# Performance work log

Hardware: AMD Instinct MI355X
Metric: run time of the kernel (lower is better)

The kernel has to match this reference:

```python
import jax, jax.numpy as jnp
import numpy as np

N = 100000   # nodes
P = 3        # metapaths
E = 800000   # edges per metapath (avg degree 8)
IN = 128     # in_size
H = 4        # layer_num_heads
D = 32       # out_size per head
HID = 64     # semantic attention hidden
NEG_SLOPE = 0.2


def setup_inputs() -> dict:
    key = jax.random.key(0)
    ks = jax.random.split(key, 10)
    h = jax.random.normal(ks[0], (N, IN), jnp.float32)
    edge_src = jax.random.randint(ks[1], (P, E), 0, N, dtype=jnp.int32).astype(jnp.int64)
    edge_dst = jax.random.randint(ks[2], (P, E), 0, N, dtype=jnp.int32).astype(jnp.int64)
    W = jax.random.normal(ks[3], (P, IN, H * D), jnp.float32) * 0.05
    attn_l = jax.random.normal(ks[4], (P, H, D), jnp.float32) * 0.05
    attn_r = jax.random.normal(ks[5], (P, H, D), jnp.float32) * 0.05
    bias = jnp.zeros((P, H * D), jnp.float32)
    sa_w1 = jax.random.normal(ks[6], (H * D, HID), jnp.float32) * 0.05
    sa_b1 = jnp.zeros((HID,), jnp.float32)
    sa_w2 = jax.random.normal(ks[7], (HID, 1), jnp.float32) * 0.05
    return {"h": h, "edge_src": edge_src, "edge_dst": edge_dst, "W": W,
            "attn_l": attn_l, "attn_r": attn_r, "bias": bias,
            "sa_w1": sa_w1, "sa_b1": sa_b1, "sa_w2": sa_w2}


def _gat_conv(h, src, dst, Wp, al, ar, bp):
    # DGL GATConv: project, per-edge additive attention, edge softmax over dst, scatter-sum.
    n = h.shape[0]
    feat = (h @ Wp).reshape(n, H, D)              # [N,H,D]
    el = (feat * al).sum(-1)                      # [N,H]
    er = (feat * ar).sum(-1)                      # [N,H]
    e = jax.nn.leaky_relu(el[src] + er[dst], NEG_SLOPE)   # [E,H]
    emax = jax.ops.segment_max(e, dst, num_segments=n)    # [N,H]
    emax = jnp.where(jnp.isfinite(emax), emax, 0.0)       # zero-in-degree guard
    ex = jnp.exp(e - emax[dst])                            # [E,H]
    denom = jax.ops.segment_sum(ex, dst, num_segments=n)   # [N,H]
    alpha = ex / jnp.maximum(denom[dst], 1e-9)              # [E,H]
    msg = alpha[:, :, None] * feat[src]                     # [E,H,D]
    out = jax.ops.segment_sum(msg, dst, num_segments=n)     # [N,H,D]
    return out.reshape(n, H * D) + bp


def reference(h, edge_src, edge_dst, W, attn_l, attn_r, bias, sa_w1, sa_b1, sa_w2):
    embs = []
    for p in range(P):  # small fixed metapath set
        embs.append(_gat_conv(h, edge_src[p], edge_dst[p], W[p], attn_l[p], attn_r[p], bias[p]))
    z = jnp.stack(embs, axis=1)                 # [N,P,H*D]
    # SemanticAttention: MLP score, mean over nodes, softmax over metapaths
    w = (jnp.tanh(z @ sa_w1 + sa_b1) @ sa_w2).mean(0)   # [P,1]
    beta = jax.nn.softmax(w, axis=0)                     # [P,1]
    return (beta[None, :, :] * z).sum(1)                 # [N,H*D]
```

## Files before the change

### kernel.cpp

```cpp
#include <hip/hip_runtime.h>
#include <hip/hip_bf16.h>
#include <math.h>

#define NN 100000
#define NP 3
#define NE 800000
#define NH 4
#define ND 32
#define HD 128
#define NHID 64

#define SLW 256
#define SBK 512
#define GB 391
#define NBLK 196
#define ECHUNK 4096
#define EPT 16
#define EMAX 2368

typedef __attribute__((ext_vector_type(8))) short short8;
typedef __attribute__((ext_vector_type(4))) float f32x4;

__device__ __forceinline__ unsigned short f2bf(float f) {
  union { float f; unsigned int u; } v; v.f = f;
  unsigned int r = v.u + 0x7FFFu + ((v.u >> 16) & 1u);
  return (unsigned short)(r >> 16);
}
__device__ __forceinline__ float bf2f(unsigned short u) {
  return __uint_as_float(((unsigned int)u) << 16);
}
__device__ __forceinline__ float tanh_fast(float x) {
  return 1.f - 2.f / (1.f + __expf(2.f * x));
}

__global__ __launch_bounds__(256) void prep_fill_kernel(
    const float* __restrict__ h, const float* __restrict__ W, const float* __restrict__ W1,
    const int* __restrict__ src_all, const int* __restrict__ dst_all,
    unsigned short* __restrict__ hb, unsigned short* __restrict__ WT,
    unsigned short* __restrict__ W1T, float* __restrict__ s,
    int* __restrict__ cntA, int* __restrict__ baseA, int* __restrict__ pairs) {
  __shared__ int hist[SBK];
  __shared__ int scanb[SBK];
  const int tid = threadIdx.x;
  const int bx = blockIdx.x;
  if (bx < 12500) {
    int i = bx * 256 + tid;
    if (i < NN * 32) {
      float4 v = ((const float4*)h)[i];
      ushort4 o;
      o.x = f2bf(v.x); o.y = f2bf(v.y); o.z = f2bf(v.z); o.w = f2bf(v.w);
      ((ushort4*)hb)[i] = o;
    }
    if (i < NP * 128 * 128) {
      int p = i >> 14, r = i & 16383, n = r >> 7, k = r & 127;
      WT[i] = f2bf(W[(size_t)p * 16384 + k * 128 + n]);
    }
    if (i < NHID * 128) {
      int n = i >> 7, k = i & 127;
      W1T[i] = f2bf(W1[(size_t)k * NHID + n]);
    }
    if (i < 4) s[i] = 0.f;
    return;
  }
  const int b2 = bx - 12500;
  const int p = b2 / NBLK, blk = b2 % NBLK;
  const int* dstp = dst_all + (size_t)p * NE;
  const int* srcp = src_all + (size_t)p * NE;
  hist[tid] = 0; hist[tid + 256] = 0;
  __syncthreads();
  int dv[EPT], sv[EPT];
#pragma unroll
  for (int k = 0; k < EPT; ++k) {
    int e = blk * ECHUNK + k * 256 + tid;
    dv[k] = -1; sv[k] = 0;
    if (e < NE) {
      dv[k] = __builtin_nontemporal_load(dstp + e);
      sv[k] = __builtin_nontemporal_load(srcp + e);
    }
    if (dv[k] >= 0) atomicAdd(&hist[(unsigned)dv[k] >> 8], 1);
  }
  __syncthreads();
  scanb[tid] = hist[tid]; scanb[tid + 256] = hist[tid + 256];
  __syncthreads();
  for (int off = 1; off < SBK; off <<= 1) {
    int a0 = (tid >= off) ? scanb[tid - off] : 0;
    int a1 = scanb[tid + 256 - off];
    __syncthreads();
    scanb[tid] += a0; scanb[tid + 256] += a1;
    __syncthreads();
  }
  int c0 = hist[tid], c1 = hist[tid + 256];
  int b0 = scanb[tid] - c0, b1 = scanb[tid + 256] - c1;
  int* cA = cntA + ((size_t)p * NBLK + blk) * SBK;
  int* bA = baseA + ((size_t)p * NBLK + blk) * SBK;
  cA[tid] = c0; cA[tid + 256] = c1;
  bA[tid] = b0; bA[tid + 256] = b1;
  __syncthreads();
  scanb[tid] = b0; scanb[tid + 256] = b1;
  hist[tid] = 0; hist[tid + 256] = 0;
  __syncthreads();
  int* prp = pairs + (size_t)p * NE + (size_t)blk * ECHUNK;
#pragma unroll
  for (int k = 0; k < EPT; ++k) {
    if (dv[k] >= 0) {
      int sl = (unsigned)dv[k] >> 8;
      int pos = scanb[sl] + atomicAdd(&hist[sl], 1);
      prp[pos] = ((dv[k] & 255) << 17) | sv[k];
    }
  }
}

__global__ __launch_bounds__(256) void gemm_mfma_kernel(
    const unsigned short* __restrict__ hb, const unsigned short* __restrict__ WT_all,
    const float* __restrict__ al_all, const float* __restrict__ ar_all,
    unsigned short* __restrict__ featb_all, float* __restrict__ el_all,
    float* __restrict__ er_all) {
  __shared__ unsigned short Bs[128 * 128];
  const int p = blockIdx.y;
  const unsigned short* WTp = WT_all + (size_t)p * 16384;
#pragma unroll
  for (int it = 0; it < 8; ++it)
    ((float4*)Bs)[it * 256 + threadIdx.x] = ((const float4*)WTp)[it * 256 + threadIdx.x];
  __syncthreads();

  const int wid = threadIdx.x >> 6, lane = threadIdx.x & 63;
  const int c = lane & 15, q = lane >> 4;
  const int tile = blockIdx.x * 4 + wid;
  const int tc = tile < 6250 ? tile : 6249;

  f32x4 acc[8];
#pragma unroll
  for (int t = 0; t < 8; ++t) acc[t] = (f32x4){0.f, 0.f, 0.f, 0.f};

  const unsigned short* arow = hb + (size_t)(tc * 16 + c) * 128 + q * 8;
#pragma unroll
  for (int kc = 0; kc < 4; ++kc) {
    short8 a = *(const short8*)(arow + kc * 32);
#pragma unroll
    for (int t = 0; t < 8; ++t) {
      short8 b = *(const short8*)(Bs + (size_t)(t * 16 + c) * 128 + kc * 32 + q * 8);
      acc[t] = __builtin_amdgcn_mfma_f32_16x16x32_bf16(a, b, acc[t], 0, 0, 0);
    }
  }
  if (tile >= 6250) return;

  unsigned short* featb = featb_all + (size_t)p * NN * 128;
#pragma unroll
  for (int t = 0; t < 8; ++t)
#pragma unroll
    for (int i = 0; i < 4; ++i)
      featb[(size_t)(tc * 16 + q * 4 + i) * 128 + t * 16 + c] = f2bf(acc[t][i]);

  const float* al = al_all + p * 128;
  const float* ar = ar_all + p * 128;
  float alv[8], arv[8];
#pragma unroll
  for (int t = 0; t < 8; ++t) { alv[t] = al[t * 16 + c]; arv[t] = ar[t * 16 + c]; }
  float elp[4][4], erp[4][4];
#pragma unroll
  for (int i = 0; i < 4; ++i)
#pragma unroll
    for (int hh = 0; hh < 4; ++hh) {
      elp[i][hh] = acc[2 * hh][i] * alv[2 * hh] + acc[2 * hh + 1][i] * alv[2 * hh + 1];
      erp[i][hh] = acc[2 * hh][i] * arv[2 * hh] + acc[2 * hh + 1][i] * arv[2 * hh + 1];
    }
#pragma unroll
  for (int m = 1; m <= 8; m <<= 1)
#pragma unroll
    for (int i = 0; i < 4; ++i)
#pragma unroll
      for (int hh = 0; hh < 4; ++hh) {
        elp[i][hh] += __shfl_xor(elp[i][hh], m);
        erp[i][hh] += __shfl_xor(erp[i][hh], m);
      }
  if (c == 0) {
    float* el = el_all + (size_t)p * NN * 4;
    float* er = er_all + (size_t)p * NN * 4;
#pragma unroll
    for (int i = 0; i < 4; ++i) {
      int row = tc * 16 + q * 4 + i;
      *(float4*)(el + (size_t)row * 4) = make_float4(elp[i][0], elp[i][1], elp[i][2], elp[i][3]);
      *(float4*)(er + (size_t)row * 4) = make_float4(erp[i][0], erp[i][1], erp[i][2], erp[i][3]);
    }
  }
}

__global__ __launch_bounds__(512) void fillB2a_kernel(
    const int* __restrict__ cntA, const int* __restrict__ baseA,
    const int* __restrict__ pairs, int* __restrict__ srtpk,
    int2* __restrict__ rowidx, int* __restrict__ btot) {
  __shared__ int scnt[NBLK];
  __shared__ int sbase[NBLK];
  __shared__ int scum[NBLK];
  __shared__ int totE;
  __shared__ int hist[SLW];
  __shared__ int start[SLW];
  __shared__ int wcur[SLW];
  __shared__ int earr[EMAX];
  const int tid = threadIdx.x;
  const int p = blockIdx.y, sl = blockIdx.x;
  const size_t base = ((size_t)p * GB + sl) * EMAX;

  for (int b = tid; b < NBLK; b += 512) {
    scnt[b] = cntA[((size_t)p * NBLK + b) * SBK + sl];
    sbase[b] = baseA[((size_t)p * NBLK + b) * SBK + sl];
  }
  if (tid < SLW) hist[tid] = 0;
  __syncthreads();
  if (tid < NBLK) scum[tid] = scnt[tid];
  __syncthreads();
  for (int off = 1; off < NBLK; off <<= 1) {
    int a = (tid < NBLK && tid >= off) ? scum[tid - off] : 0;
    __syncthreads();
    if (tid < NBLK) scum[tid] += a;
    __syncthreads();
  }
  if (tid == NBLK - 1) { int t = scum[NBLK - 1]; totE = t > EMAX ? EMAX : t; }
  int excl = (tid < NBLK) ? scum[tid] - scnt[tid] : 0;
  __syncthreads();
  if (tid < NBLK) scum[tid] = excl;
  __syncthreads();
  const int total = totE;
  const int* prp = pairs + (size_t)p * NE;
  for (int e = tid; e < total; e += 512) {
    int lo = 0, hi = NBLK - 1;
    while (lo < hi) { int mid = (lo + hi + 1) >> 1; if (scum[mid] <= e) lo = mid; else hi = mid - 1; }
    int pk = prp[(size_t)lo * ECHUNK + sbase[lo] + (e - scum[lo])];
    earr[e] = pk;
    atomicAdd(&hist[pk >> 17], 1);
  }
  __syncthreads();
  if (tid < SLW) start[tid] = hist[tid];
  __syncthreads();
  for (int off = 1; off < SLW; off <<= 1) {
    int a = (tid < SLW && tid >= off) ? start[tid - off] : 0;
    __syncthreads();
    if (tid < SLW) start[tid] += a;
    __syncthreads();
  }
  if (tid < SLW) { int st = start[tid] - hist[tid]; start[tid] = st; wcur[tid] = st; }
  __syncthreads();
  for (int e = tid; e < total; e += 512) {
    int pk = earr[e];
    int pos = atomicAdd(&wcur[pk >> 17], 1);
    srtpk[base + pos] = pk;
  }
  if (tid < SLW) {
    int n = sl * SLW + tid;
    if (n < NN) rowidx[(size_t)p * NN + n] = make_int2((int)(base + start[tid]), hist[tid]);
  }
  if (tid == 0) btot[p * GB + sl] = total;
}

__global__ __launch_bounds__(256) void fillB2b_kernel(
    const int* __restrict__ srtpk, const int* __restrict__ btot,
    const float* __restrict__ el_all, const float* __restrict__ er_all,
    float4* __restrict__ xs) {
  const int p = blockIdx.y, sl = blockIdx.x;
  const int total = btot[p * GB + sl];
  const size_t base = ((size_t)p * GB + sl) * EMAX;
  const float* el = el_all + (size_t)p * NN * 4;
  const float* er = er_all + (size_t)p * NN * 4;
  for (int i = threadIdx.x; i < total; i += 256) {
    int pk = srtpk[base + i];
    int src = pk & 0x1FFFF, dl = pk >> 17;
    int n = sl * SLW + dl;
    float4 ev = *(const float4*)(el + (size_t)src * 4);
    float4 rv = *(const float4*)(er + (size_t)n * 4);
    float4 x;
    float e0 = ev.x + rv.x; e0 = fmaxf(e0, 0.2f * e0); x.x = __expf(e0);
    float e1 = ev.y + rv.y; e1 = fmaxf(e1, 0.2f * e1); x.y = __expf(e1);
    float e2 = ev.z + rv.z; e2 = fmaxf(e2, 0.2f * e2); x.z = __expf(e2);
    float e3 = ev.w + rv.w; e3 = fmaxf(e3, 0.2f * e3); x.w = __expf(e3);
    xs[base + i] = x;
  }
}

__global__ __launch_bounds__(256) void gather3_kernel(
    const unsigned short* __restrict__ featb_all, const int* __restrict__ srtpk,
    const float* __restrict__ xs, const int2* __restrict__ rowidx,
    const float* __restrict__ bias_all, unsigned short* __restrict__ zb) {
  const int p = blockIdx.y;
  const unsigned short* featb = featb_all + (size_t)p * NN * 128;
  const int wid = threadIdx.x >> 6;
  const int lane = threadIdx.x & 63;
  const int n = blockIdx.x * 4 + wid;
  int2 rd = rowidx[(size_t)p * NN + n];
  const int rbase = rd.x, deg = rd.y;

  const int j16 = lane & 15, hgrp = lane >> 4;
  const int sub = lane >> 4, c16 = lane & 15;
  const int hh = c16 >> 2;

  float acc[8] = {0.f, 0.f, 0.f, 0.f, 0.f, 0.f, 0.f, 0.f};
  float dsum = 0.f;

  for (int b = 0; b < deg; b += 16) {
    int s = 0; float x = 0.f;
    int jj = b + j16;
    if (jj < deg) {
      int idx = rbase + jj;
      s = srtpk[idx] & 0x1FFFF;
      x = xs[(size_t)idx * 4 + hgrp];
    }
    int bend = deg - b; bend = bend > 16 ? 16 : bend;
    for (int i = 0; i < bend; i += 8) {
      int j0 = i + sub, j1 = i + 4 + sub;
      int s0 = __shfl(s, j0);
      int s1 = __shfl(s, j1);
      float xv0 = __shfl(x, (hh << 4) | j0);
      float xv1 = __shfl(x, (hh << 4) | j1);
      short8 f0 = *(const short8*)(featb + (size_t)s0 * 128 + c16 * 8);
      short8 f1 = *(const short8*)(featb + (size_t)s1 * 128 + c16 * 8);
      dsum += xv0 + xv1;
#pragma unroll
      for (int k = 0; k < 8; ++k) acc[k] += xv0 * bf2f((unsigned short)f0[k]);
#pragma unroll
      for (int k = 0; k < 8; ++k) acc[k] += xv1 * bf2f((unsigned short)f1[k]);
    }
  }
  dsum += __shfl_xor(dsum, 16); dsum += __shfl_xor(dsum, 32);
#pragma unroll
  for (int k = 0; k < 8; ++k) {
    acc[k] += __shfl_xor(acc[k], 16);
    acc[k] += __shfl_xor(acc[k], 32);
  }
  if (sub == 0) {
    float rdn = dsum > 0.f ? 1.f / dsum : 0.f;
    const float* bias = bias_all + p * 128 + c16 * 8;
    float4 b0 = *(const float4*)(bias);
    float4 b1 = *(const float4*)(bias + 4);
    short8 o;
    o[0] = f2bf(acc[0] * rdn + b0.x); o[1] = f2bf(acc[1] * rdn + b0.y);
    o[2] = f2bf(acc[2] * rdn + b0.z); o[3] = f2bf(acc[3] * rdn + b0.w);
    o[4] = f2bf(acc[4] * rdn + b1.x); o[5] = f2bf(acc[5] * rdn + b1.y);
    o[6] = f2bf(acc[6] * rdn + b1.z); o[7] = f2bf(acc[7] * rdn + b1.w);
    *(short8*)(zb + (size_t)n * (NP * 128) + p * 128 + c16 * 8) = o;
  }
}

__global__ __launch_bounds__(256) void sem_mfma_kernel(
    const unsigned short* __restrict__ zb, const unsigned short* __restrict__ W1T,
    const float* __restrict__ b1, const float* __restrict__ w2,
    float* __restrict__ s) {
  __shared__ float red3[3];
  if (threadIdx.x < 3) red3[threadIdx.x] = 0.f;
  __syncthreads();
  const int wid = threadIdx.x >> 6, lane = threadIdx.x & 63;
  const int tile = blockIdx.x * 4 + wid;
  const bool active = tile < 18750;
  const int tc = active ? tile : 18749;
  const int c = lane & 15, q = lane >> 4;
  f32x4 acc[4];
#pragma unroll
  for (int t = 0; t < 4; ++t) acc[t] = (f32x4){0.f, 0.f, 0.f, 0.f};

  const unsigned short* arow = zb + (size_t)(tc * 16 + c) * 128 + q * 8;
  const unsigned short* brow = W1T + (size_t)c * 128 + q * 8;
#pragma unroll
  for (int kc = 0; kc < 4; ++kc) {
    short8 a = *(const short8*)(arow + kc * 32);
#pragma unroll
    for (int t = 0; t < 4; ++t) {
      short8 b = *(const short8*)(brow + (size_t)t * 16 * 128 + kc * 32);
      acc[t] = __builtin_amdgcn_mfma_f32_16x16x32_bf16(a, b, acc[t], 0, 0, 0);
    }
  }
  float part[4] = {0.f, 0.f, 0.f, 0.f};
#pragma unroll
  for (int t = 0; t < 4; ++t) {
    float bb = b1[t * 16 + c], ww = w2[t * 16 + c];
#pragma unroll
    for (int i = 0; i < 4; ++i) part[i] += tanh_fast(acc[t][i] + bb) * ww;
  }
#pragma unroll
  for (int m = 1; m <= 8; m <<= 1)
#pragma unroll
    for (int i = 0; i < 4; ++i) part[i] += __shfl_xor(part[i], m);
  if (active && c == 0) {
#pragma unroll
    for (int i = 0; i < 4; ++i)
      atomicAdd(&red3[(tc * 16 + q * 4 + i) % 3], part[i]);
  }
  __syncthreads();
  if (threadIdx.x < 3) atomicAdd(&s[threadIdx.x], red3[threadIdx.x]);
}

__global__ __launch_bounds__(256) void final_kernel(
    const unsigned short* __restrict__ zb, const float* __restrict__ s,
    float* __restrict__ out) {
  int i = blockIdx.x * blockDim.x + threadIdx.x;
  if (i >= NN * 16) return;
  float w0 = s[0] * (1.f / NN), w1 = s[1] * (1.f / NN), w2c = s[2] * (1.f / NN);
  float m = fmaxf(w0, fmaxf(w1, w2c));
  float e0 = __expf(w0 - m), e1 = __expf(w1 - m), e2 = __expf(w2c - m);
  float inv = 1.f / (e0 + e1 + e2);
  float b0 = e0 * inv, b1 = e1 * inv, b2 = e2 * inv;
  int n = i >> 4, g = i & 15;
  const unsigned short* zr = zb + (size_t)n * (NP * 128) + g * 8;
  ushort4 u0a = *(const ushort4*)(zr);
  ushort4 u0b = *(const ushort4*)(zr + 4);
  ushort4 u1a = *(const ushort4*)(zr + 128);
  ushort4 u1b = *(const ushort4*)(zr + 132);
  ushort4 u2a = *(const ushort4*)(zr + 256);
  ushort4 u2b = *(const ushort4*)(zr + 260);
  float4 oa, ob;
  oa.x = b0 * bf2f(u0a.x) + b1 * bf2f(u1a.x) + b2 * bf2f(u2a.x);
  oa.y = b0 * bf2f(u0a.y) + b1 * bf2f(u1a.y) + b2 * bf2f(u2a.y);
  oa.z = b0 * bf2f(u0a.z) + b1 * bf2f(u1a.z) + b2 * bf2f(u2a.z);
  oa.w = b0 * bf2f(u0a.w) + b1 * bf2f(u1a.w) + b2 * bf2f(u2a.w);
  ob.x = b0 * bf2f(u0b.x) + b1 * bf2f(u1b.x) + b2 * bf2f(u2b.x);
  ob.y = b0 * bf2f(u0b.y) + b1 * bf2f(u1b.y) + b2 * bf2f(u2b.y);
  ob.z = b0 * bf2f(u0b.z) + b1 * bf2f(u1b.z) + b2 * bf2f(u2b.z);
  ob.w = b0 * bf2f(u0b.w) + b1 * bf2f(u1b.w) + b2 * bf2f(u2b.w);
  float* op = out + (size_t)n * 128 + g * 8;
  *(float4*)op = oa;
  *(float4*)(op + 4) = ob;
}

extern "C" void kernel_launch(void* const* d_in, const int* in_sizes, int n_in,
                              void* d_out, int out_size, void* d_ws, size_t ws_size,
                              hipStream_t stream) {
  const float* h    = (const float*)d_in[0];
  const int*   esrc = (const int*)d_in[1];
  const int*   edst = (const int*)d_in[2];
  const float* W    = (const float*)d_in[3];
  const float* al   = (const float*)d_in[4];
  const float* ar   = (const float*)d_in[5];
  const float* bias = (const float*)d_in[6];
  const float* w1   = (const float*)d_in[7];
  const float* b1   = (const float*)d_in[8];
  const float* w2   = (const float*)d_in[9];
  float* out = (float*)d_out;

  unsigned short* zb    = (unsigned short*)d_ws;
  unsigned short* featb = zb + (size_t)38400000;
  unsigned short* WT    = featb + (size_t)38400000;
  unsigned short* W1T   = WT + 49152;
  float* el   = (float*)(W1T + 8192);
  float* er   = el + (size_t)1200000;
  float* s    = er + (size_t)1200000;
  int2* rowidx = (int2*)(s + 16);
  int* btot  = (int*)(rowidx + (size_t)NP * NN);
  int* srtpk = btot + 1280;
  int* cntA  = srtpk + (size_t)NP * GB * EMAX;
  int* baseA = cntA + (size_t)NP * NBLK * SBK;
  int* pairs = baseA + (size_t)NP * NBLK * SBK;
  unsigned short* hb = (unsigned short*)(pairs + (size_t)NP * NE);
  float* xs = (float*)cntA;

  prep_fill_kernel<<<12500 + NP * NBLK, 256, 0, stream>>>(
      h, W, w1, esrc, edst, hb, WT, W1T, s, cntA, baseA, pairs);

  dim3 bGrid(GB, NP);
  fillB2a_kernel<<<bGrid, 512, 0, stream>>>(cntA, baseA, pairs, srtpk, rowidx, btot);

  dim3 gemmGrid(NN / 64 + 1, NP);
  gemm_mfma_kernel<<<gemmGrid, 256, 0, stream>>>(hb, WT, al, ar, featb, el, er);

  fillB2b_kernel<<<bGrid, 256, 0, stream>>>(srtpk, btot, el, er, (float4*)xs);

  dim3 gatherGrid(NN / 4, NP);
  gather3_kernel<<<gatherGrid, 256, 0, stream>>>(featb, srtpk, xs, rowidx, bias, zb);

  sem_mfma_kernel<<<(18750 + 3) / 4, 256, 0, stream>>>(zb, W1T, b1, w2, s);
  final_kernel<<<(NN * 16 + 255) / 256, 256, 0, stream>>>(zb, s, out);
}
```

Before: 457.5 us.

## Map one node per 16-lane group in gather kernel instead of one per wavefront

The gather/aggregation kernel now assigns each destination node to a 16-thread group (4 nodes per wavefront, 16 per block) rather than a full 64-lane wavefront. Each thread loads the edge index and weight itself in a 4-way unrolled loop, which removes the shuffles and the cross-lane reduction at the end. The aim is to cut wasted lanes on the average degree of 8 and the reduction overhead. In exchange, nodes within one wavefront have different degrees, so lanes diverge, and each lane issues its own redundant scalar loads of the index and weight.

```diff
diff --git a/kernel.cpp b/kernel.cpp
--- a/kernel.cpp
+++ b/kernel.cpp
@@ -276,67 +276,48 @@
   }
 }
 
-__global__ __launch_bounds__(256) void gather3_kernel(
+__global__ __launch_bounds__(256) void gather4_kernel(
     const unsigned short* __restrict__ featb_all, const int* __restrict__ srtpk,
     const float* __restrict__ xs, const int2* __restrict__ rowidx,
     const float* __restrict__ bias_all, unsigned short* __restrict__ zb) {
   const int p = blockIdx.y;
   const unsigned short* featb = featb_all + (size_t)p * NN * 128;
-  const int wid = threadIdx.x >> 6;
-  const int lane = threadIdx.x & 63;
-  const int n = blockIdx.x * 4 + wid;
+  const int q = threadIdx.x >> 4;
+  const int c16 = threadIdx.x & 15;
+  const int hh = c16 >> 2;
+  const int n = blockIdx.x * 16 + q;
   int2 rd = rowidx[(size_t)p * NN + n];
   const int rbase = rd.x, deg = rd.y;
 
-  const int j16 = lane & 15, hgrp = lane >> 4;
-  const int sub = lane >> 4, c16 = lane & 15;
-  const int hh = c16 >> 2;
-
   float acc[8] = {0.f, 0.f, 0.f, 0.f, 0.f, 0.f, 0.f, 0.f};
   float dsum = 0.f;
 
-  for (int b = 0; b < deg; b += 16) {
-    int s = 0; float x = 0.f;
-    int jj = b + j16;
-    if (jj < deg) {
+  for (int j = 0; j < deg; j += 4) {
+#pragma unroll
+    for (int u = 0; u < 4; ++u) {
+      int jj = j + u;
+      bool v = jj < deg;
       int idx = rbase + jj;
-      s = srtpk[idx] & 0x1FFFF;
-      x = xs[(size_t)idx * 4 + hgrp];
-    }
-    int bend = deg - b; bend = bend > 16 ? 16 : bend;
-    for (int i = 0; i < bend; i += 8) {
-      int j0 = i + sub, j1 = i + 4 + sub;
-      int s0 = __shfl(s, j0);
-      int s1 = __shfl(s, j1);
-      float xv0 = __shfl(x, (hh << 4) | j0);
-      float xv1 = __shfl(x, (hh << 4) | j1);
-      short8 f0 = *(const short8*)(featb + (size_t)s0 * 128 + c16 * 8);
-      short8 f1 = *(const short8*)(featb + (size_t)s1 * 128 + c16 * 8);
-      dsum += xv0 + xv1;
-#pragma unroll
-      for (int k = 0; k < 8; ++k) acc[k] += xv0 * bf2f((unsigned short)f0[k]);
-#pragma unroll
-      for (int k = 0; k < 8; ++k) acc[k] += xv1 * bf2f((unsigned short)f1[k]);
-    }
-  }
-  dsum += __shfl_xor(dsum, 16); dsum += __shfl_xor(dsum, 32);
-#pragma unroll
-  for (int k = 0; k < 8; ++k) {
-    acc[k] += __shfl_xor(acc[k], 16);
-    acc[k] += __shfl_xor(acc[k], 32);
-  }
-  if (sub == 0) {
-    float rdn = dsum > 0.f ? 1.f / dsum : 0.f;
-    const float* bias = bias_all + p * 128 + c16 * 8;
-    float4 b0 = *(const float4*)(bias);
-    float4 b1 = *(const float4*)(bias + 4);
-    short8 o;
-    o[0] = f2bf(acc[0] * rdn + b0.x); o[1] = f2bf(acc[1] * rdn + b0.y);
-    o[2] = f2bf(acc[2] * rdn + b0.z); o[3] = f2bf(acc[3] * rdn + b0.w);
-    o[4] = f2bf(acc[4] * rdn + b1.x); o[5] = f2bf(acc[5] * rdn + b1.y);
-    o[6] = f2bf(acc[6] * rdn + b1.z); o[7] = f2bf(acc[7] * rdn + b1.w);
-    *(short8*)(zb + (size_t)n * (NP * 128) + p * 128 + c16 * 8) = o;
-  }
+      int pk = v ? srtpk[idx] : 0;
+      float x = v ? xs[(size_t)idx * 4 + hh] : 0.f;
+      int s = pk & 0x1FFFF;
+      short8 f = *(const short8*)(featb + (size_t)s * 128 + c16 * 8);
+      dsum += x;
+#pragma unroll
+      for (int k = 0; k < 8; ++k) acc[k] += x * bf2f((unsigned short)f[k]);
+    }
+  }
+
+  float rdn = dsum > 0.f ? 1.f / dsum : 0.f;
+  const float* bias = bias_all + p * 128 + c16 * 8;
+  float4 b0 = *(const float4*)(bias);
+  float4 b1 = *(const float4*)(bias + 4);
+  short8 o;
+  o[0] = f2bf(acc[0] * rdn + b0.x); o[1] = f2bf(acc[1] * rdn + b0.y);
+  o[2] = f2bf(acc[2] * rdn + b0.z); o[3] = f2bf(acc[3] * rdn + b0.w);
+  o[4] = f2bf(acc[4] * rdn + b1.x); o[5] = f2bf(acc[5] * rdn + b1.y);
+  o[6] = f2bf(acc[6] * rdn + b1.z); o[7] = f2bf(acc[7] * rdn + b1.w);
+  *(short8*)(zb + (size_t)n * (NP * 128) + p * 128 + c16 * 8) = o;
 }
 
 __global__ __launch_bounds__(256) void sem_mfma_kernel(
@@ -460,8 +441,8 @@
 
   fillB2b_kernel<<<bGrid, 256, 0, stream>>>(srtpk, btot, el, er, (float4*)xs);
 
-  dim3 gatherGrid(NN / 4, NP);
-  gather3_kernel<<<gatherGrid, 256, 0, stream>>>(featb, srtpk, xs, rowidx, bias, zb);
+  dim3 gatherGrid(NN / 16, NP);
+  gather4_kernel<<<gatherGrid, 256, 0, stream>>>(featb, srtpk, xs, rowidx, bias, zb);
 
   sem_mfma_kernel<<<(18750 + 3) / 4, 256, 0, stream>>>(zb, W1T, b1, w2, s);
   final_kernel<<<(NN * 16 + 255) / 256, 256, 0, stream>>>(zb, s, out);
```

After: 446.3 us. -2.5%, faster.
